# Kernel optimization log

Measured on AMD Instinct MI355X. Metric: run time of the kernel, lower is better.

The kernel has to match this reference:

```python
import jax, jax.numpy as jnp
import numpy as np

FILTER_SIZE = 1024
NUM_HEADS = 16
D_HEAD = FILTER_SIZE // NUM_HEADS
LN_EPS = 1e-5


def setup_inputs() -> dict:
    key = jax.random.key(0)
    ks = jax.random.split(key, 10)
    B, T, D = 2, 2048, FILTER_SIZE
    s = 1.0 / np.sqrt(D)
    return {
        "x": jax.random.normal(ks[0], (B, T, D), dtype=jnp.float32),
        "Wq": jax.random.normal(ks[1], (D, D), dtype=jnp.float32) * s,
        "bq": jnp.zeros((D,), dtype=jnp.float32),
        "Wk": jax.random.normal(ks[2], (D, D), dtype=jnp.float32) * s,
        "bk": jnp.zeros((D,), dtype=jnp.float32),
        "Wv": jax.random.normal(ks[3], (D, D), dtype=jnp.float32) * s,
        "bv": jnp.zeros((D,), dtype=jnp.float32),
        "Wo": jax.random.normal(ks[4], (D, D), dtype=jnp.float32) * s,
        "bo": jnp.zeros((D,), dtype=jnp.float32),
        "gamma": jnp.ones((D,), dtype=jnp.float32),
        "beta": jnp.zeros((D,), dtype=jnp.float32),
    }


def reference(x, Wq, bq, Wk, bk, Wv, bv, Wo, bo, gamma, beta):
    B, T, D = x.shape
    H, Dh = NUM_HEADS, D_HEAD
    # Note: source splits features as (d_head, heads) with heads LAST.
    q = (x @ Wq.T + bq).reshape(B, T, Dh, H)
    k = (x @ Wk.T + bk).reshape(B, T, Dh, H)
    v = (x @ Wv.T + bv).reshape(B, T, Dh, H)
    scale = 1.0 / np.sqrt(Dh).astype(np.float32)
    # scores: (B, H, T, T)
    scores = jnp.einsum("bidh,bjdh->bhij", q, k) * scale
    attn = jax.nn.softmax(scores, axis=-1)  # dropout is identity in eval
    out = jnp.einsum("bhij,bjdh->bidh", attn, v)  # (B, T, Dh, H)
    out = out.reshape(B, T, D)  # matches permute(0,2,3,1).reshape in torch
    out = out @ Wo.T + bo
    out = out + x
    mu = jnp.mean(out, axis=-1, keepdims=True)
    var = jnp.var(out, axis=-1, keepdims=True)
    out = (out - mu) * jax.lax.rsqrt(var + LN_EPS) * gamma + beta
    return out
```

## Files before the change

### kernel.cpp

```cpp
#include <hip/hip_runtime.h>
#include <stdint.h>

#define T_SEQ 2048
#define D_MODEL 1024
#define NH 16
#define DH 64
#define NROWS 4096

typedef __bf16 bf16x8 __attribute__((ext_vector_type(8)));
typedef float floatx4 __attribute__((ext_vector_type(4)));
typedef short short4v __attribute__((ext_vector_type(4)));
typedef short short8v __attribute__((ext_vector_type(8)));

#define AS1 __attribute__((address_space(1)))
#define AS3 __attribute__((address_space(3)))

static __device__ __forceinline__ void gl2lds16(const unsigned short* g, unsigned short* s) {
    __builtin_amdgcn_global_load_lds((const AS1 unsigned int*)g, (AS3 unsigned int*)s, 16, 0, 0);
}

static __device__ __forceinline__ unsigned short f32_bf16(float f) {
    union { float f; unsigned int u; } c; c.f = f;
    unsigned int u = c.u;
    u = u + 0x7FFFu + ((u >> 16) & 1u);
    return (unsigned short)(u >> 16);
}

static __device__ __forceinline__ unsigned int pack2_bf16(float a, float b) {
    return (unsigned int)f32_bf16(a) | ((unsigned int)f32_bf16(b) << 16);
}

static __device__ __forceinline__ floatx4 mfma16(bf16x8 a, bf16x8 b, floatx4 c) {
    return __builtin_amdgcn_mfma_f32_16x16x32_bf16(a, b, c, 0, 0, 0);
}

static __device__ __forceinline__ floatx4 mfma16k16(short4v a, short4v b, floatx4 c) {
#if defined(__HIP_DEVICE_COMPILE__)
    return __builtin_amdgcn_mfma_f32_16x16x16bf16_1k(a, b, c, 0, 0, 0);
#else
    (void)a; (void)b;
    return c;
#endif
}

#define QSCALE 0.1803368801111204f
#define EXP2_SHIFT 10.0f

__global__ __launch_bounds__(256) void k_conv_all(const float* __restrict__ x,
                                                  const float* __restrict__ Wq,
                                                  const float* __restrict__ Wk,
                                                  const float* __restrict__ Wv,
                                                  const float* __restrict__ Wo,
                                                  unsigned short* __restrict__ x_bf,
                                                  unsigned short* __restrict__ wqkv_bf,
                                                  unsigned short* __restrict__ wo_bf) {
    int b = blockIdx.x, t = threadIdx.x;
    if (b < 4096) {
        int i = b * 1024 + t * 4;
        float4 v = *(const float4*)(x + i);
        uint2 o;
        o.x = pack2_bf16(v.x, v.y);
        o.y = pack2_bf16(v.z, v.w);
        *(uint2*)(x_bf + i) = o;
    } else if (b < 7168) {
        int idx = b - 4096;
        int tensor = idx >> 10, np = idx & 1023;
        const float* src = tensor == 0 ? Wq : tensor == 1 ? Wk : Wv;
        int f = (np & 63) * 16 + (np >> 6);
        int c = t * 4;
        float4 v = *(const float4*)(src + (long)f * D_MODEL + c);
        uint2 o;
        o.x = pack2_bf16(v.x, v.y);
        o.y = pack2_bf16(v.z, v.w);
        *(uint2*)(wqkv_bf + ((long)tensor * D_MODEL + np) * D_MODEL + c) = o;
    } else {
        int n = b - 7168;
        int fp = t * 4;
        const float* row = Wo + (long)n * D_MODEL;
        unsigned short o[4];
        #pragma unroll
        for (int k = 0; k < 4; k++) {
            int f = fp + k;
            o[k] = f32_bf16(row[(f & 63) * 16 + (f >> 6)]);
        }
        *(uint2*)(wo_bf + (long)n * D_MODEL + fp) = *(const uint2*)o;
    }
}

template <int BN, int MODE>
__global__ __launch_bounds__(256) void k_gemm(const unsigned short* __restrict__ A,
                                              const unsigned short* __restrict__ W,
                                              const float* __restrict__ b0,
                                              const float* __restrict__ b1,
                                              const float* __restrict__ b2,
                                              const float* __restrict__ resid,
                                              unsigned short* __restrict__ out_bf,
                                              unsigned short* __restrict__ vtg,
                                              float* __restrict__ out_f32) {
    constexpr int NT = BN / 32;
    constexpr int NCB = BN / 32;
    __shared__ unsigned short lds_a[128 * 64];
    __shared__ unsigned short lds_b[BN * 64];
    const int tid = threadIdx.x;
    const int w = tid >> 6, l = tid & 63;
    const int lrow = l & 15, lq = l >> 4;
    const int wm = (w >> 1) * 64, wn = (w & 1) * (BN / 2);
    const int L = blockIdx.x;
    const int bx = (L & 7) * 4 + ((L >> 3) & 3);
    const int by = L >> 5;
    const long am0 = (long)bx * 128;
    const long wn0 = (long)by * BN;

    floatx4 acc[4][NT] = {};
    const int grow = l >> 3;
    const int gcol = ((l & 7) ^ grow) * 8;
    const int sw8 = (lrow & 7);

    for (int k0 = 0; k0 < D_MODEL; k0 += 64) {
        #pragma unroll
        for (int c = 0; c < 4; c++) {
            int chunk = w * 4 + c;
            gl2lds16(A + (am0 + chunk * 8 + grow) * D_MODEL + k0 + gcol,
                     lds_a + chunk * 512);
        }
        #pragma unroll
        for (int c = 0; c < NCB; c++) {
            int chunk = w * NCB + c;
            gl2lds16(W + (wn0 + chunk * 8 + grow) * D_MODEL + k0 + gcol,
                     lds_b + chunk * 512);
        }
        __syncthreads();

        bf16x8 af[4][2], bf[NT][2];
        #pragma unroll
        for (int mt = 0; mt < 4; mt++)
            #pragma unroll
            for (int ks = 0; ks < 2; ks++)
                af[mt][ks] = *(const bf16x8*)(lds_a + (wm + mt * 16 + lrow) * 64 +
                                              (((ks * 4 + lq) ^ sw8) * 8));
        #pragma unroll
        for (int nt = 0; nt < NT; nt++)
            #pragma unroll
            for (int ks = 0; ks < 2; ks++)
                bf[nt][ks] = *(const bf16x8*)(lds_b + (wn + nt * 16 + lrow) * 64 +
                                              (((ks * 4 + lq) ^ sw8) * 8));
        #pragma unroll
        for (int mt = 0; mt < 4; mt++)
            #pragma unroll
            for (int nt = 0; nt < NT; nt++)
                #pragma unroll
                for (int ks = 0; ks < 2; ks++)
                    acc[mt][nt] = mfma16(af[mt][ks], bf[nt][ks], acc[mt][nt]);
        __syncthreads();
    }

    if (MODE == 0) {
        int tensor = by >> 3;
        int nbase = (by & 7) * 128;
        const float* bias = tensor == 0 ? b0 : tensor == 1 ? b1 : b2;
        float scale = tensor == 0 ? QSCALE : 1.0f;
        if (tensor < 2) {
            unsigned short* outt = out_bf + (size_t)tensor * (32u * T_SEQ * DH);
            #pragma unroll
            for (int mt = 0; mt < 4; mt++) {
                #pragma unroll
                for (int nt = 0; nt < NT; nt++) {
                    int n = nbase + wn + nt * 16 + lrow;
                    int h = n >> 6, d = n & 63;
                    float bb = bias[d * 16 + h];
                    #pragma unroll
                    for (int r = 0; r < 4; r++) {
                        int row = (int)am0 + wm + mt * 16 + lq * 4 + r;
                        float v = (acc[mt][nt][r] + bb) * scale;
                        int b = row >> 11, i = row & 2047;
                        long idx = ((long)(b * 16 + h) * T_SEQ + i) * DH + d;
                        outt[idx] = f32_bf16(v);
                    }
                }
            }
        } else {
            int row0 = (int)am0 + wm;
            int b = row0 >> 11;
            int blk = (row0 & 2047) >> 6;
            #pragma unroll
            for (int nt = 0; nt < NT; nt++) {
                int n = nbase + wn + nt * 16 + lrow;
                int h = n >> 6, d = n & 63;
                float bb = bias[d * 16 + h];
                long base = (((long)(b * 16 + h) * 64 + d) * 32 + blk) * 64;
                #pragma unroll
                for (int mt = 0; mt < 4; mt++) {
                    uint2 o;
                    o.x = pack2_bf16(acc[mt][nt][0] + bb, acc[mt][nt][1] + bb);
                    o.y = pack2_bf16(acc[mt][nt][2] + bb, acc[mt][nt][3] + bb);
                    *(uint2*)(vtg + base + lq * 16 + mt * 4) = o;
                }
            }
        }
    } else {
        #pragma unroll
        for (int mt = 0; mt < 4; mt++) {
            #pragma unroll
            for (int nt = 0; nt < NT; nt++) {
                int n = (int)wn0 + wn + nt * 16 + lrow;
                float bb = b0[n];
                #pragma unroll
                for (int r = 0; r < 4; r++) {
                    int row = (int)am0 + wm + mt * 16 + lq * 4 + r;
                    long idx = (long)row * D_MODEL + n;
                    out_f32[idx] = acc[mt][nt][r] + bb + resid[idx];
                }
            }
        }
    }
}

#define PAD 72
__global__ __launch_bounds__(256) void k_attn(const unsigned short* __restrict__ q_ws,
                                              const unsigned short* __restrict__ k_ws,
                                              const unsigned short* __restrict__ vtg,
                                              unsigned short* __restrict__ att) {
    __shared__ unsigned short lds_k[64 * PAD];
    __shared__ unsigned short lds_v[64 * PAD];
    const int tid = threadIdx.x;
    const int w = tid >> 6, l = tid & 63;
    const int lrow = l & 15, lq = l >> 4;
    const int L = blockIdx.x;
    const int bh = (L & 7) * 4 + ((L >> 3) & 3);
    const int i0 = (L >> 5) * 128;
    const unsigned short* kh = k_ws + (long)bh * T_SEQ * DH;
    const unsigned short* vh = vtg + (long)bh * 64 * T_SEQ;

    bf16x8 qf[2][2];
    #pragma unroll
    for (int qt = 0; qt < 2; qt++) {
        const unsigned short* qp =
            q_ws + ((long)bh * T_SEQ + i0 + w * 32 + qt * 16 + lrow) * DH + lq * 8;
        qf[qt][0] = *(const bf16x8*)qp;
        qf[qt][1] = *(const bf16x8*)(qp + 32);
    }
    floatx4 o_acc[2][4] = {};
    floatx4 l_acc[2] = {};
    const short4v ones = {0x3F80, 0x3F80, 0x3F80, 0x3F80};

    const int srow = tid >> 3, scol = (tid & 7) * 8;
    for (int jt = 0; jt < T_SEQ / 64; jt++) {
        int j0 = jt * 64;
        __syncthreads();
        *(uint4*)(lds_k + srow * PAD + scol) = *(const uint4*)(kh + (long)(j0 + srow) * DH + scol);
        *(uint4*)(lds_k + (srow + 32) * PAD + scol) = *(const uint4*)(kh + (long)(j0 + srow + 32) * DH + scol);
        *(uint4*)(lds_v + srow * PAD + scol) = *(const uint4*)(vh + ((long)srow * 32 + jt) * 64 + scol);
        *(uint4*)(lds_v + (srow + 32) * PAD + scol) = *(const uint4*)(vh + ((long)(srow + 32) * 32 + jt) * 64 + scol);
        __syncthreads();

        floatx4 s0[4], s1[4];
        #pragma unroll
        for (int nt = 0; nt < 4; nt++) {
            const unsigned short* kp = lds_k + (nt * 16 + lrow) * PAD + lq * 8;
            bf16x8 ka = *(const bf16x8*)kp;
            bf16x8 kb = *(const bf16x8*)(kp + 32);
            floatx4 c0 = {-EXP2_SHIFT, -EXP2_SHIFT, -EXP2_SHIFT, -EXP2_SHIFT};
            floatx4 c1 = c0;
            c0 = mfma16(ka, qf[0][0], c0);
            c0 = mfma16(kb, qf[0][1], c0);
            c1 = mfma16(ka, qf[1][0], c1);
            c1 = mfma16(kb, qf[1][1], c1);
            s0[nt] = c0;
            s1[nt] = c1;
        }
        short4v pf0[4], pf1[4];
        #pragma unroll
        for (int nt = 0; nt < 4; nt++) {
            {
                float p0 = __builtin_amdgcn_exp2f(s0[nt][0]);
                float p1 = __builtin_amdgcn_exp2f(s0[nt][1]);
                float p2 = __builtin_amdgcn_exp2f(s0[nt][2]);
                float p3 = __builtin_amdgcn_exp2f(s0[nt][3]);
                uint2 pk;
                pk.x = __builtin_amdgcn_perm(__float_as_uint(p1), __float_as_uint(p0), 0x07060302);
                pk.y = __builtin_amdgcn_perm(__float_as_uint(p3), __float_as_uint(p2), 0x07060302);
                union { uint2 u; short4v s4; } cv; cv.u = pk;
                pf0[nt] = cv.s4;
                l_acc[0] = mfma16k16(ones, pf0[nt], l_acc[0]);
            }
            {
                float p0 = __builtin_amdgcn_exp2f(s1[nt][0]);
                float p1 = __builtin_amdgcn_exp2f(s1[nt][1]);
                float p2 = __builtin_amdgcn_exp2f(s1[nt][2]);
                float p3 = __builtin_amdgcn_exp2f(s1[nt][3]);
                uint2 pk;
                pk.x = __builtin_amdgcn_perm(__float_as_uint(p1), __float_as_uint(p0), 0x07060302);
                pk.y = __builtin_amdgcn_perm(__float_as_uint(p3), __float_as_uint(p2), 0x07060302);
                union { uint2 u; short4v s4; } cv; cv.u = pk;
                pf1[nt] = cv.s4;
                l_acc[1] = mfma16k16(ones, pf1[nt], l_acc[1]);
            }
        }
        #pragma unroll
        for (int dt = 0; dt < 4; dt++) {
            const unsigned short* vp = lds_v + (dt * 16 + lrow) * PAD + lq * 16;
            short8v v01 = *(const short8v*)vp;
            short8v v23 = *(const short8v*)(vp + 8);
            short4v va = __builtin_shufflevector(v01, v01, 0, 1, 2, 3);
            short4v vb = __builtin_shufflevector(v01, v01, 4, 5, 6, 7);
            short4v vc = __builtin_shufflevector(v23, v23, 0, 1, 2, 3);
            short4v vd = __builtin_shufflevector(v23, v23, 4, 5, 6, 7);
            o_acc[0][dt] = mfma16k16(va, pf0[0], o_acc[0][dt]);
            o_acc[0][dt] = mfma16k16(vb, pf0[1], o_acc[0][dt]);
            o_acc[0][dt] = mfma16k16(vc, pf0[2], o_acc[0][dt]);
            o_acc[0][dt] = mfma16k16(vd, pf0[3], o_acc[0][dt]);
            o_acc[1][dt] = mfma16k16(va, pf1[0], o_acc[1][dt]);
            o_acc[1][dt] = mfma16k16(vb, pf1[1], o_acc[1][dt]);
            o_acc[1][dt] = mfma16k16(vc, pf1[2], o_acc[1][dt]);
            o_acc[1][dt] = mfma16k16(vd, pf1[3], o_acc[1][dt]);
        }
    }
    int h = bh & 15, b = bh >> 4;
    #pragma unroll
    for (int qt = 0; qt < 2; qt++) {
        float rl = 1.0f / l_acc[qt][0];
        int i = i0 + w * 32 + qt * 16 + lrow;
        unsigned short* orow = att + ((long)(b * T_SEQ + i)) * D_MODEL + h * 64;
        #pragma unroll
        for (int dt = 0; dt < 4; dt++) {
            uint2 o;
            o.x = pack2_bf16(o_acc[qt][dt][0] * rl, o_acc[qt][dt][1] * rl);
            o.y = pack2_bf16(o_acc[qt][dt][2] * rl, o_acc[qt][dt][3] * rl);
            *(uint2*)(orow + dt * 16 + lq * 4) = o;
        }
    }
}

__global__ __launch_bounds__(256) void k_ln(float* __restrict__ io,
                                            const float* __restrict__ gamma,
                                            const float* __restrict__ beta) {
    int row = blockIdx.x, t = threadIdx.x;
    float* p = io + (long)row * D_MODEL + t * 4;
    float4 v = *(float4*)p;
    float s = v.x + v.y + v.z + v.w;
    float ss = v.x * v.x + v.y * v.y + v.z * v.z + v.w * v.w;
    #pragma unroll
    for (int m = 1; m < 64; m <<= 1) {
        s += __shfl_xor(s, m);
        ss += __shfl_xor(ss, m);
    }
    __shared__ float red[8];
    if ((t & 63) == 0) { red[t >> 6] = s; red[4 + (t >> 6)] = ss; }
    __syncthreads();
    s = red[0] + red[1] + red[2] + red[3];
    ss = red[4] + red[5] + red[6] + red[7];
    float mu = s * (1.0f / 1024.0f);
    float var = ss * (1.0f / 1024.0f) - mu * mu;
    float rstd = rsqrtf(var + 1e-5f);
    float4 g = *(const float4*)(gamma + t * 4);
    float4 be = *(const float4*)(beta + t * 4);
    float4 o;
    o.x = (v.x - mu) * rstd * g.x + be.x;
    o.y = (v.y - mu) * rstd * g.y + be.y;
    o.z = (v.z - mu) * rstd * g.z + be.z;
    o.w = (v.w - mu) * rstd * g.w + be.w;
    *(float4*)p = o;
}

extern "C" void kernel_launch(void* const* d_in, const int* in_sizes, int n_in,
                              void* d_out, int out_size, void* d_ws, size_t ws_size,
                              hipStream_t stream) {
    const float* x = (const float*)d_in[0];
    const float* Wq = (const float*)d_in[1];
    const float* bq = (const float*)d_in[2];
    const float* Wk = (const float*)d_in[3];
    const float* bk = (const float*)d_in[4];
    const float* Wv = (const float*)d_in[5];
    const float* bv = (const float*)d_in[6];
    const float* Wo = (const float*)d_in[7];
    const float* bo = (const float*)d_in[8];
    const float* gamma = (const float*)d_in[9];
    const float* beta = (const float*)d_in[10];
    float* out = (float*)d_out;

    char* ws = (char*)d_ws;
    unsigned short* x_bf = (unsigned short*)(ws);
    unsigned short* wqkv_bf = (unsigned short*)(ws + ((size_t)8 << 20));
    unsigned short* wo_bf = (unsigned short*)(ws + ((size_t)14 << 20));
    unsigned short* qkv_ws = (unsigned short*)(ws + ((size_t)16 << 20));
    unsigned short* att = x_bf;

    unsigned short* q_ws = qkv_ws;
    unsigned short* k_ws = qkv_ws + (size_t)32 * T_SEQ * DH;
    unsigned short* vtg = qkv_ws + (size_t)64 * T_SEQ * DH;

    k_conv_all<<<8192, 256, 0, stream>>>(x, Wq, Wk, Wv, Wo, x_bf, wqkv_bf, wo_bf);

    k_gemm<128, 0><<<768, 256, 0, stream>>>(
        x_bf, wqkv_bf, bq, bk, bv, nullptr, qkv_ws, vtg, nullptr);

    k_attn<<<512, 256, 0, stream>>>(q_ws, k_ws, vtg, att);

    k_gemm<64, 1><<<512, 256, 0, stream>>>(
        att, wo_bf, bo, nullptr, nullptr, x, nullptr, nullptr, out);

    k_ln<<<NROWS, 256, 0, stream>>>(out, gamma, beta);
}
```

Baseline: 218.8 us.

## Double-buffer attention K/V tiles via async global-to-LDS loads with XOR swizzle

Result: no change. 215.6 us (-1.4%).

```diff
diff --git a/kernel.cpp b/kernel.cpp
--- a/kernel.cpp
+++ b/kernel.cpp
@@ -45,6 +45,8 @@
 
 #define QSCALE 0.1803368801111204f
 #define EXP2_SHIFT 10.0f
+#define WAITCNT_VM4 0x0F74
+#define WAITCNT_VM0 0x0F70
 
 __global__ __launch_bounds__(256) void k_conv_all(const float* __restrict__ x,
                                                   const float* __restrict__ Wq,
@@ -215,21 +217,24 @@
     }
 }
 
-#define PAD 72
 __global__ __launch_bounds__(256) void k_attn(const unsigned short* __restrict__ q_ws,
                                               const unsigned short* __restrict__ k_ws,
                                               const unsigned short* __restrict__ vtg,
                                               unsigned short* __restrict__ att) {
-    __shared__ unsigned short lds_k[64 * PAD];
-    __shared__ unsigned short lds_v[64 * PAD];
+    __shared__ unsigned short kbuf[2 * 64 * 64];
+    __shared__ unsigned short vbuf[2 * 64 * 64];
     const int tid = threadIdx.x;
     const int w = tid >> 6, l = tid & 63;
     const int lrow = l & 15, lq = l >> 4;
+    const int sw = lrow & 7;
     const int L = blockIdx.x;
     const int bh = (L & 7) * 4 + ((L >> 3) & 3);
     const int i0 = (L >> 5) * 128;
     const unsigned short* kh = k_ws + (long)bh * T_SEQ * DH;
     const unsigned short* vh = vtg + (long)bh * 64 * T_SEQ;
+
+    const int rl = l >> 3;
+    const int gl = ((l & 7) ^ rl) * 8;
 
     bf16x8 qf[2][2];
     #pragma unroll
@@ -243,22 +248,38 @@
     floatx4 l_acc[2] = {};
     const short4v ones = {0x3F80, 0x3F80, 0x3F80, 0x3F80};
 
-    const int srow = tid >> 3, scol = (tid & 7) * 8;
+    auto stage = [&](int jt, int sel) {
+        unsigned short* kd = kbuf + sel * 4096 + (w * 2) * 512;
+        unsigned short* vd = vbuf + sel * 4096 + (w * 2) * 512;
+        #pragma unroll
+        for (int c = 0; c < 2; c++) {
+            int row = w * 16 + c * 8 + rl;
+            gl2lds16(kh + ((long)(jt * 64 + row)) * 64 + gl, kd + c * 512);
+            gl2lds16(vh + ((long)row * 32 + jt) * 64 + gl, vd + c * 512);
+        }
+    };
+
+    stage(0, 0);
+
     for (int jt = 0; jt < T_SEQ / 64; jt++) {
-        int j0 = jt * 64;
-        __syncthreads();
-        *(uint4*)(lds_k + srow * PAD + scol) = *(const uint4*)(kh + (long)(j0 + srow) * DH + scol);
-        *(uint4*)(lds_k + (srow + 32) * PAD + scol) = *(const uint4*)(kh + (long)(j0 + srow + 32) * DH + scol);
-        *(uint4*)(lds_v + srow * PAD + scol) = *(const uint4*)(vh + ((long)srow * 32 + jt) * 64 + scol);
-        *(uint4*)(lds_v + (srow + 32) * PAD + scol) = *(const uint4*)(vh + ((long)(srow + 32) * 32 + jt) * 64 + scol);
-        __syncthreads();
+        const int cur = jt & 1;
+        if (jt < T_SEQ / 64 - 1) {
+            stage(jt + 1, 1 - cur);
+            __builtin_amdgcn_s_waitcnt(WAITCNT_VM4);
+        } else {
+            __builtin_amdgcn_s_waitcnt(WAITCNT_VM0);
+        }
+        __builtin_amdgcn_s_barrier();
+
+        const unsigned short* kb_ = kbuf + cur * 4096;
+        const unsigned short* vb_ = vbuf + cur * 4096;
 
         floatx4 s0[4], s1[4];
         #pragma unroll
         for (int nt = 0; nt < 4; nt++) {
-            const unsigned short* kp = lds_k + (nt * 16 + lrow) * PAD + lq * 8;
-            bf16x8 ka = *(const bf16x8*)kp;
-            bf16x8 kb = *(const bf16x8*)(kp + 32);
+            const unsigned short* kp = kb_ + (nt * 16 + lrow) * 64;
+            bf16x8 ka = *(const bf16x8*)(kp + ((lq ^ sw) * 8));
+            bf16x8 kb = *(const bf16x8*)(kp + (((lq + 4) ^ sw) * 8));
             floatx4 c0 = {-EXP2_SHIFT, -EXP2_SHIFT, -EXP2_SHIFT, -EXP2_SHIFT};
             floatx4 c1 = c0;
             c0 = mfma16(ka, qf[0][0], c0);
@@ -298,9 +319,9 @@
         }
         #pragma unroll
         for (int dt = 0; dt < 4; dt++) {
-            const unsigned short* vp = lds_v + (dt * 16 + lrow) * PAD + lq * 16;
-            short8v v01 = *(const short8v*)vp;
-            short8v v23 = *(const short8v*)(vp + 8);
+            const unsigned short* vp = vb_ + (dt * 16 + lrow) * 64;
+            short8v v01 = *(const short8v*)(vp + (((2 * lq) ^ sw) * 8));
+            short8v v23 = *(const short8v*)(vp + (((2 * lq + 1) ^ sw) * 8));
             short4v va = __builtin_shufflevector(v01, v01, 0, 1, 2, 3);
             short4v vb = __builtin_shufflevector(v01, v01, 4, 5, 6, 7);
             short4v vc = __builtin_shufflevector(v23, v23, 0, 1, 2, 3);
@@ -314,18 +335,19 @@
             o_acc[1][dt] = mfma16k16(vc, pf1[2], o_acc[1][dt]);
             o_acc[1][dt] = mfma16k16(vd, pf1[3], o_acc[1][dt]);
         }
+        __syncthreads();
     }
     int h = bh & 15, b = bh >> 4;
     #pragma unroll
     for (int qt = 0; qt < 2; qt++) {
-        float rl = 1.0f / l_acc[qt][0];
+        float rl2 = 1.0f / l_acc[qt][0];
         int i = i0 + w * 32 + qt * 16 + lrow;
         unsigned short* orow = att + ((long)(b * T_SEQ + i)) * D_MODEL + h * 64;
         #pragma unroll
         for (int dt = 0; dt < 4; dt++) {
             uint2 o;
-            o.x = pack2_bf16(o_acc[qt][dt][0] * rl, o_acc[qt][dt][1] * rl);
-            o.y = pack2_bf16(o_acc[qt][dt][2] * rl, o_acc[qt][dt][3] * rl);
+            o.x = pack2_bf16(o_acc[qt][dt][0] * rl2, o_acc[qt][dt][1] * rl2);
+            o.y = pack2_bf16(o_acc[qt][dt][2] * rl2, o_acc[qt][dt][3] * rl2);
             *(uint2*)(orow + dt * 16 + lq * 4) = o;
         }
     }
```
